# Kernel tuning notes

Measured on AMD Instinct MI355X. Metric: run time of the kernel, lower is better.

Reference implementation:

```python
import jax, jax.numpy as jnp
import numpy as np
import math

B, N, DIM = 4, 4096, 1024
HEADS, DHEAD, NRF = 16, 64, 64
STAB = 1e-6  # numerical_stabilizer


def setup_inputs() -> dict:
    key = jax.random.key(0)
    k1, k2, k3, k4 = jax.random.split(key, 4)
    x = jax.random.normal(k1, (B, N, DIM), dtype=jnp.float32)
    W_qkv = jax.random.normal(k2, (DIM, 3 * HEADS * DHEAD), dtype=jnp.float32) * (1.0 / math.sqrt(DIM))
    RF = jax.random.normal(k3, (HEADS, DHEAD, NRF), dtype=jnp.float32) / math.sqrt(NRF)
    W_out = jax.random.normal(k4, (HEADS * DHEAD, DIM), dtype=jnp.float32) * (1.0 / math.sqrt(HEADS * DHEAD))
    b_out = jnp.zeros((DIM,), dtype=jnp.float32)
    return {"x": x, "W_qkv": W_qkv, "RF": RF, "W_out": W_out, "b_out": b_out}


def _phi(t, RF):
    # kernel transformation: project onto random features, then ReLU (default kernel)
    return jax.nn.relu(jnp.einsum('bhnd,hdr->bhnr', t, RF))


def reference(x, W_qkv, RF, W_out, b_out):
    b, n, _ = x.shape
    qkv = x @ W_qkv                                  # [b, n, 3*h*d]
    q, k, v = jnp.split(qkv, 3, axis=-1)
    def to_heads(t):
        return t.reshape(b, n, HEADS, DHEAD).transpose(0, 2, 1, 3)  # [b,h,n,d]
    q, k, v = to_heads(q), to_heads(k), to_heads(v)

    phi_q = _phi(q, RF)                              # [b,h,n,r]
    phi_k = _phi(k, RF)                              # [b,h,n,r]

    # linear-complexity FAVOR+ attention
    kv = jnp.einsum('bhnr,bhnd->bhrd', phi_k, v)     # [b,h,r,d]
    out = jnp.einsum('bhnr,bhrd->bhnd', phi_q, kv)   # [b,h,n,d]
    # normalizer: einsum('bhnr,bhmr->bhn') == phi_q @ sum_m(phi_k)
    k_sum = phi_k.sum(axis=2)                        # [b,h,r]
    normalizer = jnp.einsum('bhnr,bhr->bhn', phi_q, k_sum)[..., None] + STAB
    out = out / normalizer

    out = out.transpose(0, 2, 1, 3).reshape(b, n, HEADS * DHEAD)
    out = out @ W_out + b_out
    return out
```

## Files before the change

### kernel.cpp

```cpp
#include <hip/hip_runtime.h>


typedef __attribute__((ext_vector_type(8))) short s8v;
typedef __attribute__((ext_vector_type(4))) short s4v;
typedef __attribute__((ext_vector_type(4))) float f4v;
typedef __attribute__((ext_vector_type(4))) int   i4v;

#define MFMA16(a, b, c) __builtin_amdgcn_mfma_f32_16x16x32_bf16((a), (b), (c), 0, 0, 0)

__device__ __forceinline__ unsigned short f2bf(float f) {
  unsigned int u = __builtin_bit_cast(unsigned int, f);
  unsigned int r = (u + 0x7FFFu + ((u >> 16) & 1u)) >> 16;
  return (unsigned short)r;
}

__device__ __forceinline__ int swz(int p) {
  return p ^ (((p >> 7) & 7) << 4);
}
__device__ __forceinline__ int swz8(int p) {
  return p ^ (((p >> 8) & 7) << 4);
}

__device__ __forceinline__ void gl_lds16(const void* g, void* l) {
  __builtin_amdgcn_global_load_lds(
      (const __attribute__((address_space(1))) void*)g,
      (__attribute__((address_space(3))) void*)l, 16, 0, 0);
}

__global__ __launch_bounds__(256) void cvt_bf16(const float* __restrict__ in,
                                                unsigned short* __restrict__ out,
                                                int n4) {
  int i = blockIdx.x * 256 + threadIdx.x;
  if (i >= n4) return;
  f4v v = ((const f4v*)in)[i];
  s4v o;
#pragma unroll
  for (int j = 0; j < 4; ++j) o[j] = (short)f2bf(v[j]);
  ((s4v*)out)[i] = o;
}

__global__ __launch_bounds__(256) void transpose_cvt(const float* __restrict__ in,
                                                     unsigned short* __restrict__ out,
                                                     int R, int C) {
  __shared__ float tile[32][33];
  const int tx = threadIdx.x, ty = threadIdx.y;
  const int c0 = blockIdx.x * 32, r0 = blockIdx.y * 32;
#pragma unroll
  for (int j = 0; j < 4; ++j)
    tile[ty + j * 8][tx] = in[(size_t)(r0 + ty + j * 8) * C + c0 + tx];
  __syncthreads();
#pragma unroll
  for (int j = 0; j < 4; ++j)
    out[(size_t)(c0 + ty + j * 8) * R + r0 + tx] = f2bf(tile[tx][ty + j * 8]);
}

__global__ __launch_bounds__(256) void fold_w(const float* __restrict__ W_qkv,
                                              const float* __restrict__ RF,
                                              unsigned short* __restrict__ wqkvt) {
  __shared__ float RFl[64 * 64];
  __shared__ float Wl[128 * 65];
  const int t = threadIdx.x;
  const int k0 = blockIdx.x * 128, h = blockIdx.y, part = blockIdx.z;
#pragma unroll
  for (int i = 0; i < 16; ++i) RFl[i * 256 + t] = RF[h * 4096 + i * 256 + t];
#pragma unroll
  for (int i = 0; i < 32; ++i) {
    int idx = i * 256 + t, kk = idx >> 6, d = idx & 63;
    Wl[kk * 65 + d] = W_qkv[(size_t)(k0 + kk) * 3072 + part * 1024 + h * 64 + d];
  }
  __syncthreads();
  const int w = t >> 6, lane = t & 63;
  const int rg = w >> 1;
  const int kk = (w & 1) * 64 + lane;
#pragma unroll
  for (int j = 0; j < 32; ++j) {
    const int r = rg * 32 + j;
    float s = 0.f;
#pragma unroll
    for (int d = 0; d < 64; ++d) s += Wl[kk * 65 + d] * RFl[d * 64 + r];
    wqkvt[(size_t)(part * 1024 + h * 64 + r) * 1024 + k0 + kk] = f2bf(s);
  }
}

template <int MODE>
__global__ __launch_bounds__(512, 2) void gemm256(const unsigned short* __restrict__ A,
                                                  const unsigned short* __restrict__ Bt,
                                                  void* __restrict__ Cout,
                                                  unsigned short* __restrict__ kT,
                                                  unsigned short* __restrict__ vT,
                                                  const float* __restrict__ bias,
                                                  int Nn, int K, int NTN, int CPX) {
  __shared__ __align__(128) unsigned short smem[65536];
  const int t = threadIdx.x, w = t >> 6, lane = t & 63;
  const int wm = w >> 2, wn = w & 3;
  const int fr = lane & 15, c16 = (lane >> 4) * 16;
  const int nkt = K >> 6;

  const int bid = blockIdx.x;
  const int wg = (bid & 7) * CPX + (bid >> 3);
  const int tm = wg / NTN, tn = wg % NTN;

  const unsigned short* gA = A + (size_t)tm * 256 * K;
  const unsigned short* gB = Bt + (size_t)tn * 256 * K;

  const int s0 = swz(t * 16);
  const int s1 = swz(8192 + t * 16);
  const int goff0 = (s0 >> 7) * K + ((s0 & 127) >> 1);
  const int goff1 = ((s1 - 8192) >> 7) * K + ((s1 & 127) >> 1) + 64 * K;
  const int woff = w * 1024;

  auto stage = [&](int T2, int part) {
    if (T2 >= nkt) return;
    char* reg = (char*)smem + (((T2 & 1) * 4 + part) << 14);
    const unsigned short* gp =
        (part < 2 ? gA : gB) + (size_t)((part & 1) * 128) * K + T2 * 64;
    gl_lds16(gp + goff0, reg + woff);
    gl_lds16(gp + goff1, reg + 8192 + woff);
  };

  f4v acc[8][4] = {};
  stage(0, 0); stage(0, 1); stage(0, 2); stage(0, 3);

  auto rdA = [&](int mh, s8v (&a)[4][2], const char* Ar) {
#pragma unroll
    for (int i = 0; i < 4; ++i)
#pragma unroll
      for (int ks = 0; ks < 2; ++ks) {
        int p = swz((mh * 64 + i * 16 + fr) * 128 + ks * 64 + c16);
        a[i][ks] = *(const s8v*)(Ar + p);
      }
  };
  auto rdB = [&](int nh, s8v (&b)[2][2], const char* Br, int brow) {
#pragma unroll
    for (int j = 0; j < 2; ++j)
#pragma unroll
      for (int ks = 0; ks < 2; ++ks) {
        int p = swz((brow + nh * 32 + j * 16 + fr) * 128 + ks * 64 + c16);
        b[j][ks] = *(const s8v*)(Br + p);
      }
  };
  auto mmac = [&](int mh, int nh, const s8v (&a)[4][2], const s8v (&b)[2][2]) {
    __builtin_amdgcn_s_setprio(1);
#pragma unroll
    for (int i = 0; i < 4; ++i)
#pragma unroll
      for (int j = 0; j < 2; ++j) {
        acc[mh * 4 + i][nh * 2 + j] = MFMA16(a[i][0], b[j][0], acc[mh * 4 + i][nh * 2 + j]);
        acc[mh * 4 + i][nh * 2 + j] = MFMA16(a[i][1], b[j][1], acc[mh * 4 + i][nh * 2 + j]);
      }
    __builtin_amdgcn_s_setprio(0);
  };

  const int brow = (wn & 1) * 64;
  for (int T = 0; T < nkt; ++T) {
    const int d = T & 1;
    const char* Ar = (const char*)smem + ((d * 4 + wm) << 14);
    const char* Br = (const char*)smem + ((d * 4 + 2 + (wn >> 1)) << 14);
    asm volatile("s_waitcnt vmcnt(0)" ::: "memory");
    __builtin_amdgcn_s_barrier();
    __builtin_amdgcn_sched_barrier(0);
    stage(T + 1, 0); stage(T + 1, 1); stage(T + 1, 2); stage(T + 1, 3);
    s8v a[4][2], b0[2][2], b1[2][2];
    rdA(0, a, Ar); rdB(0, b0, Br, brow); rdB(1, b1, Br, brow);
    mmac(0, 0, a, b0);
    mmac(0, 1, a, b1);
    rdA(1, a, Ar);
    mmac(1, 1, a, b1);
    mmac(1, 0, a, b0);
  }

  const int sec = tn >> 2;
#pragma unroll
  for (int m = 0; m < 8; ++m)
#pragma unroll
    for (int n = 0; n < 4; ++n) {
      const int row = tm * 256 + wm * 128 + m * 16 + (lane >> 4) * 4;
      const int col = tn * 256 + wn * 64 + n * 16 + fr;
      if (MODE == 0) {
        if (sec == 0) {
          unsigned short* C = (unsigned short*)Cout;
#pragma unroll
          for (int r = 0; r < 4; ++r)
            C[(size_t)(row + r) * 1024 + col] = f2bf(fmaxf(acc[m][n][r], 0.0f));
        } else {
          const int cl = col & 1023;
          const int bh = (row >> 12) * 16 + (cl >> 6);
          unsigned short* T = (sec == 1) ? kT : vT;
          s4v o;
#pragma unroll
          for (int g = 0; g < 4; ++g)
            o[g] = (short)f2bf(sec == 1 ? fmaxf(acc[m][n][g], 0.0f) : acc[m][n][g]);
          *(s4v*)&T[((size_t)bh * 64 + (cl & 63)) * 4096 + (row & 4095)] = o;
        }
      } else {
        float* C = (float*)Cout;
        const float bv = bias[col];
#pragma unroll
        for (int r = 0; r < 4; ++r)
          C[(size_t)(row + r) * Nn + col] = acc[m][n][r] + bv;
      }
    }
}

__global__ __launch_bounds__(256) void kv_gemm(const unsigned short* __restrict__ kT,
                                               const unsigned short* __restrict__ vT,
                                               float* __restrict__ kvpart) {
  __shared__ __align__(128) char lds[2 * 36864];
  const int t = threadIdx.x, w = t >> 6, lane = t & 63;
  const int och = blockIdx.x, bh = blockIdx.y;
  const int fr = lane & 15, c16 = (lane >> 4) * 16;
  const char* kTb = (const char*)kT + (size_t)bh * 64 * 8192 + och * 1024;
  const char* vTb = (const char*)vT + (size_t)bh * 64 * 8192 + och * 1024;

  for (int i = t; i < 2 * 2048; i += 256) {
    int buf = i >> 11, e = i & 2047;
    int row = 64 + (e >> 7), c = e & 127;
    int p = swz8(row * 256 + c * 2);
    *(unsigned short*)&lds[buf * 36864 + 16384 + p] = (row == 64) ? 0x3F80 : 0;
  }

  int srcoff[4];
#pragma unroll
  for (int i = 0; i < 4; ++i) {
    int p = swz8((i * 256 + t) * 16);
    srcoff[i] = (p >> 8) * 8192 + (p & 255);
  }
  auto stage = [&](int s) {
    if (s >= 4) return;
    char* base = lds + (s & 1) * 36864;
#pragma unroll
    for (int i = 0; i < 4; ++i) {
      gl_lds16(kTb + s * 256 + srcoff[i], base + (i * 256 + w * 64) * 16);
      gl_lds16(vTb + s * 256 + srcoff[i], base + 16384 + (i * 256 + w * 64) * 16);
    }
  };

  f4v kvacc[5] = {};
  stage(0);
  for (int s = 0; s < 4; ++s) {
    asm volatile("s_waitcnt vmcnt(0)" ::: "memory");
    __builtin_amdgcn_s_barrier();
    __builtin_amdgcn_sched_barrier(0);
    stage(s + 1);
    const char* kB = lds + (s & 1) * 36864;
    const char* vB = kB + 16384;
    s8v a[4];
#pragma unroll
    for (int ks = 0; ks < 4; ++ks)
      a[ks] = *(const s8v*)(kB + swz8((w * 16 + fr) * 256 + ks * 64 + c16));
    __builtin_amdgcn_s_setprio(1);
#pragma unroll
    for (int f = 0; f < 5; ++f) {
#pragma unroll
      for (int ks = 0; ks < 4; ++ks) {
        s8v b = *(const s8v*)(vB + swz8((f * 16 + fr) * 256 + ks * 64 + c16));
        kvacc[f] = MFMA16(a[ks], b, kvacc[f]);
      }
    }
    __builtin_amdgcn_s_setprio(0);
  }
  float* outp = kvpart + ((size_t)bh * 8 + och) * (80 * 64);
#pragma unroll
  for (int f = 0; f < 5; ++f)
    *(f4v*)&outp[(f * 16 + fr) * 64 + w * 16 + (lane >> 4) * 4] = kvacc[f];
}

__global__ __launch_bounds__(256) void kv_reduce(const float* __restrict__ kvpart,
                                                 unsigned short* __restrict__ kvt) {
  const int bh = blockIdx.x, t = threadIdx.x;
  for (int i = t; i < 80 * 64; i += 256) {
    float s = 0.f;
#pragma unroll
    for (int c = 0; c < 8; ++c) s += kvpart[((size_t)bh * 8 + c) * 5120 + i];
    kvt[(size_t)bh * 5120 + i] = f2bf(s);
  }
}

__global__ __launch_bounds__(256) void phiq_out(const unsigned short* __restrict__ phiq,
                                                const unsigned short* __restrict__ kvt,
                                                unsigned short* __restrict__ attno) {
  __shared__ __align__(128) unsigned short phl[128 * 64];
  __shared__ unsigned short kvl[80 * 72];
  const int t = threadIdx.x, w = t >> 6, lane = t & 63;
  const int ch = blockIdx.x, h = blockIdx.y, b = blockIdx.z;
  const int fr = lane & 15, kg = (lane >> 4) * 8, c16 = (lane >> 4) * 16;
  const int bh = b * 16 + h;
  const size_t rowbase = (size_t)(b * 4096 + ch * 128);
  const char* src = (const char*)phiq + rowbase * 2048 + h * 128;

#pragma unroll
  for (int i = 0; i < 4; ++i) {
    int p = swz((i * 256 + t) * 16);
    gl_lds16(src + (p >> 7) * 2048 + (p & 127),
             (char*)phl + (i * 256 + w * 64) * 16);
  }
  for (int i = t; i < 640; i += 256) {
    int row = i >> 3, cg = (i & 7) * 8;
    *(i4v*)&kvl[row * 72 + cg] = *(const i4v*)&kvt[(size_t)bh * 5120 + row * 64 + cg];
  }
  __syncthreads();

  f4v acc[2][5] = {};
#pragma unroll
  for (int ks = 0; ks < 2; ++ks) {
    s8v pa[2], kb[5];
#pragma unroll
    for (int m = 0; m < 2; ++m)
      pa[m] = *(const s8v*)((const char*)phl +
                            swz((w * 32 + m * 16 + fr) * 128 + ks * 64 + c16));
#pragma unroll
    for (int f = 0; f < 5; ++f)
      kb[f] = *(const s8v*)&kvl[(f * 16 + fr) * 72 + ks * 32 + kg];
#pragma unroll
    for (int m = 0; m < 2; ++m)
#pragma unroll
      for (int f = 0; f < 5; ++f) acc[m][f] = MFMA16(pa[m], kb[f], acc[m][f]);
  }
#pragma unroll
  for (int m = 0; m < 2; ++m)
#pragma unroll
    for (int g = 0; g < 4; ++g) {
      float nrm = __shfl(acc[m][4][g], lane & 48) + 1e-6f;
      int n = w * 32 + m * 16 + (lane >> 4) * 4 + g;
      size_t orow = rowbase + n;
#pragma unroll
      for (int f = 0; f < 4; ++f)
        attno[orow * 1024 + h * 64 + f * 16 + fr] = f2bf(acc[m][f][g] / nrm);
    }
}

extern "C" void kernel_launch(void* const* d_in, const int* in_sizes, int n_in,
                              void* d_out, int out_size, void* d_ws, size_t ws_size,
                              hipStream_t stream) {
  const float* x = (const float*)d_in[0];
  const float* W_qkv = (const float*)d_in[1];
  const float* RF = (const float*)d_in[2];
  const float* W_out = (const float*)d_in[3];
  const float* b_out = (const float*)d_in[4];
  float* out = (float*)d_out;

  char* ws = (char*)d_ws;
  size_t off = 0;
  auto alloc = [&](size_t bytes) -> void* {
    void* p = ws + off;
    off += (bytes + 255) & ~(size_t)255;
    return p;
  };
  unsigned short* xb = (unsigned short*)alloc(16384ull * 1024 * 2);
  unsigned short* wqkvt = (unsigned short*)alloc(3072ull * 1024 * 2);
  unsigned short* woutt = (unsigned short*)alloc(1024ull * 1024 * 2);
  unsigned short* phiq = (unsigned short*)alloc(16384ull * 1024 * 2);
  unsigned short* kT = (unsigned short*)alloc(64ull * 64 * 4096 * 2);
  unsigned short* vT = (unsigned short*)alloc(64ull * 64 * 4096 * 2);
  float* kvpart = (float*)alloc(64ull * 8 * 80 * 64 * 4);
  unsigned short* kvt = (unsigned short*)alloc(64ull * 80 * 64 * 2);
  unsigned short* attno = (unsigned short*)alloc(16384ull * 1024 * 2);

  cvt_bf16<<<16384, 256, 0, stream>>>(x, xb, 4194304);
  transpose_cvt<<<dim3(96, 32), dim3(32, 8), 0, stream>>>(W_qkv, wqkvt, 1024, 3072);
  transpose_cvt<<<dim3(32, 32), dim3(32, 8), 0, stream>>>(W_out, woutt, 1024, 1024);
  fold_w<<<dim3(8, 16, 2), 256, 0, stream>>>(W_qkv, RF, wqkvt);

  gemm256<0><<<768, 512, 0, stream>>>(xb, wqkvt, phiq, kT, vT, nullptr,
                                      3072, 1024, 12, 96);
  kv_gemm<<<dim3(8, 64), 256, 0, stream>>>(kT, vT, kvpart);
  kv_reduce<<<64, 256, 0, stream>>>(kvpart, kvt);
  phiq_out<<<dim3(32, 16, 4), 256, 0, stream>>>(phiq, kvt, attno);
  gemm256<1><<<256, 512, 0, stream>>>(attno, woutt, out, nullptr, nullptr, b_out,
                                      1024, 1024, 4, 32);
}
```

Before: 260.4 us.

## Store QKV GEMM output row-major and transpose phi_k/v in kv kernel via LDS

The QKV GEMM epilogue no longer scatters phi_k and v into transposed per-head buffers. It now writes all three sections row-major into one combined buffer, with ReLU applied to the first two sections. The kv kernel now loads phi_k and v rows from that buffer into registers and transposes them through padded LDS before the MFMA. This replaces the async global-to-LDS double-buffered pipeline with synchronous loads and scalar LDS transposes. The transpose_cvt launch for W_qkv is also narrowed to the v columns, since fold_w overwrites the q/k parts.

After: 256.9 us. Within noise of the previous version (-1.4%).

```diff
diff --git a/kernel.cpp b/kernel.cpp
--- a/kernel.cpp
+++ b/kernel.cpp
@@ -16,9 +16,6 @@
 
 __device__ __forceinline__ int swz(int p) {
   return p ^ (((p >> 7) & 7) << 4);
-}
-__device__ __forceinline__ int swz8(int p) {
-  return p ^ (((p >> 8) & 7) << 4);
 }
 
 __device__ __forceinline__ void gl_lds16(const void* g, void* l) {
@@ -86,8 +83,6 @@
 __global__ __launch_bounds__(512, 2) void gemm256(const unsigned short* __restrict__ A,
                                                   const unsigned short* __restrict__ Bt,
                                                   void* __restrict__ Cout,
-                                                  unsigned short* __restrict__ kT,
-                                                  unsigned short* __restrict__ vT,
                                                   const float* __restrict__ bias,
                                                   int Nn, int K, int NTN, int CPX) {
   __shared__ __align__(128) unsigned short smem[65536];
@@ -169,7 +164,7 @@
     mmac(1, 0, a, b0);
   }
 
-  const int sec = tn >> 2;
+  const bool rel = (MODE == 0) && (tn < 8);
 #pragma unroll
   for (int m = 0; m < 8; ++m)
 #pragma unroll
@@ -177,20 +172,11 @@
       const int row = tm * 256 + wm * 128 + m * 16 + (lane >> 4) * 4;
       const int col = tn * 256 + wn * 64 + n * 16 + fr;
       if (MODE == 0) {
-        if (sec == 0) {
-          unsigned short* C = (unsigned short*)Cout;
-#pragma unroll
-          for (int r = 0; r < 4; ++r)
-            C[(size_t)(row + r) * 1024 + col] = f2bf(fmaxf(acc[m][n][r], 0.0f));
-        } else {
-          const int cl = col & 1023;
-          const int bh = (row >> 12) * 16 + (cl >> 6);
-          unsigned short* T = (sec == 1) ? kT : vT;
-          s4v o;
-#pragma unroll
-          for (int g = 0; g < 4; ++g)
-            o[g] = (short)f2bf(sec == 1 ? fmaxf(acc[m][n][g], 0.0f) : acc[m][n][g]);
-          *(s4v*)&T[((size_t)bh * 64 + (cl & 63)) * 4096 + (row & 4095)] = o;
+        unsigned short* C = (unsigned short*)Cout;
+#pragma unroll
+        for (int r = 0; r < 4; ++r) {
+          float v = acc[m][n][r];
+          C[(size_t)(row + r) * Nn + col] = f2bf(rel ? fmaxf(v, 0.0f) : v);
         }
       } else {
         float* C = (float*)Cout;
@@ -202,67 +188,62 @@
     }
 }
 
-__global__ __launch_bounds__(256) void kv_gemm(const unsigned short* __restrict__ kT,
-                                               const unsigned short* __restrict__ vT,
+__global__ __launch_bounds__(256) void phik_kv(const unsigned short* __restrict__ phib,
                                                float* __restrict__ kvpart) {
-  __shared__ __align__(128) char lds[2 * 36864];
+  __shared__ unsigned short pkt[64 * 136];
+  __shared__ unsigned short vt[80 * 136];
   const int t = threadIdx.x, w = t >> 6, lane = t & 63;
-  const int och = blockIdx.x, bh = blockIdx.y;
-  const int fr = lane & 15, c16 = (lane >> 4) * 16;
-  const char* kTb = (const char*)kT + (size_t)bh * 64 * 8192 + och * 1024;
-  const char* vTb = (const char*)vT + (size_t)bh * 64 * 8192 + och * 1024;
-
-  for (int i = t; i < 2 * 2048; i += 256) {
-    int buf = i >> 11, e = i & 2047;
-    int row = 64 + (e >> 7), c = e & 127;
-    int p = swz8(row * 256 + c * 2);
-    *(unsigned short*)&lds[buf * 36864 + 16384 + p] = (row == 64) ? 0x3F80 : 0;
-  }
-
-  int srcoff[4];
-#pragma unroll
-  for (int i = 0; i < 4; ++i) {
-    int p = swz8((i * 256 + t) * 16);
-    srcoff[i] = (p >> 8) * 8192 + (p & 255);
-  }
-  auto stage = [&](int s) {
-    if (s >= 4) return;
-    char* base = lds + (s & 1) * 36864;
-#pragma unroll
-    for (int i = 0; i < 4; ++i) {
-      gl_lds16(kTb + s * 256 + srcoff[i], base + (i * 256 + w * 64) * 16);
-      gl_lds16(vTb + s * 256 + srcoff[i], base + 16384 + (i * 256 + w * 64) * 16);
-    }
-  };
+  const int och = blockIdx.x, h = blockIdx.y, b = blockIdx.z;
+  const int fr = lane & 15, kg = (lane >> 4) * 8;
+
+  for (int i = t; i < 136; i += 256) vt[64 * 136 + i] = 0x3F80;
+  for (int i = t; i < 15 * 136; i += 256) vt[65 * 136 + i] = 0;
 
   f4v kvacc[5] = {};
-  stage(0);
-  for (int s = 0; s < 4; ++s) {
-    asm volatile("s_waitcnt vmcnt(0)" ::: "memory");
-    __builtin_amdgcn_s_barrier();
-    __builtin_amdgcn_sched_barrier(0);
-    stage(s + 1);
-    const char* kB = lds + (s & 1) * 36864;
-    const char* vB = kB + 16384;
-    s8v a[4];
-#pragma unroll
-    for (int ks = 0; ks < 4; ++ks)
-      a[ks] = *(const s8v*)(kB + swz8((w * 16 + fr) * 256 + ks * 64 + c16));
-    __builtin_amdgcn_s_setprio(1);
-#pragma unroll
-    for (int f = 0; f < 5; ++f) {
-#pragma unroll
-      for (int ks = 0; ks < 4; ++ks) {
-        s8v b = *(const s8v*)(vB + swz8((f * 16 + fr) * 256 + ks * 64 + c16));
-        kvacc[f] = MFMA16(a[ks], b, kvacc[f]);
-      }
-    }
-    __builtin_amdgcn_s_setprio(0);
-  }
+  for (int c = 0; c < 4; ++c) {
+    const size_t rowbase = (size_t)(b * 4096 + och * 512 + c * 128);
+    i4v kreg[4], vreg[4];
+#pragma unroll
+    for (int it = 0; it < 4; ++it) {
+      int slot = it * 256 + t;
+      const unsigned short* rp =
+          &phib[(rowbase + (slot >> 3)) * 3072 + h * 64 + (slot & 7) * 8];
+      kreg[it] = *(const i4v*)(rp + 1024);
+      vreg[it] = *(const i4v*)(rp + 2048);
+    }
+    __syncthreads();
+#pragma unroll
+    for (int it = 0; it < 4; ++it) {
+      int slot = it * 256 + t;
+      int vn = slot >> 3, c8 = (slot & 7) * 8;
+      const unsigned short* kr = (const unsigned short*)&kreg[it];
+      const unsigned short* vr = (const unsigned short*)&vreg[it];
+#pragma unroll
+      for (int j = 0; j < 8; ++j) {
+        pkt[(c8 + j) * 136 + vn] = kr[j];
+        vt[(c8 + j) * 136 + vn] = vr[j];
+      }
+    }
+    __syncthreads();
+#pragma unroll
+    for (int kst = 0; kst < 4; ++kst) {
+      s8v pb = *(const s8v*)&pkt[(w * 16 + fr) * 136 + kst * 32 + kg];
+#pragma unroll
+      for (int f = 0; f < 5; ++f) {
+        s8v va = *(const s8v*)&vt[(f * 16 + fr) * 136 + kst * 32 + kg];
+        kvacc[f] = MFMA16(va, pb, kvacc[f]);
+      }
+    }
+  }
+  const int bh = b * 16 + h;
   float* outp = kvpart + ((size_t)bh * 8 + och) * (80 * 64);
 #pragma unroll
-  for (int f = 0; f < 5; ++f)
-    *(f4v*)&outp[(f * 16 + fr) * 64 + w * 16 + (lane >> 4) * 4] = kvacc[f];
+  for (int f = 0; f < 5; ++f) {
+    int row = f * 16 + (lane >> 4) * 4;
+    int col = w * 16 + fr;
+#pragma unroll
+    for (int g = 0; g < 4; ++g) outp[(row + g) * 64 + col] = kvacc[f][g];
+  }
 }
 
 __global__ __launch_bounds__(256) void kv_reduce(const float* __restrict__ kvpart,
@@ -276,7 +257,7 @@
   }
 }
 
-__global__ __launch_bounds__(256) void phiq_out(const unsigned short* __restrict__ phiq,
+__global__ __launch_bounds__(256) void phiq_out(const unsigned short* __restrict__ phib,
                                                 const unsigned short* __restrict__ kvt,
                                                 unsigned short* __restrict__ attno) {
   __shared__ __align__(128) unsigned short phl[128 * 64];
@@ -286,12 +267,12 @@
   const int fr = lane & 15, kg = (lane >> 4) * 8, c16 = (lane >> 4) * 16;
   const int bh = b * 16 + h;
   const size_t rowbase = (size_t)(b * 4096 + ch * 128);
-  const char* src = (const char*)phiq + rowbase * 2048 + h * 128;
+  const char* src = (const char*)phib + rowbase * 6144 + h * 128;
 
 #pragma unroll
   for (int i = 0; i < 4; ++i) {
     int p = swz((i * 256 + t) * 16);
-    gl_lds16(src + (p >> 7) * 2048 + (p & 127),
+    gl_lds16(src + (p >> 7) * 6144 + (p & 127),
              (char*)phl + (i * 256 + w * 64) * 16);
   }
   for (int i = t; i < 640; i += 256) {
@@ -349,23 +330,20 @@
   unsigned short* xb = (unsigned short*)alloc(16384ull * 1024 * 2);
   unsigned short* wqkvt = (unsigned short*)alloc(3072ull * 1024 * 2);
   unsigned short* woutt = (unsigned short*)alloc(1024ull * 1024 * 2);
-  unsigned short* phiq = (unsigned short*)alloc(16384ull * 1024 * 2);
-  unsigned short* kT = (unsigned short*)alloc(64ull * 64 * 4096 * 2);
-  unsigned short* vT = (unsigned short*)alloc(64ull * 64 * 4096 * 2);
+  unsigned short* phib = (unsigned short*)alloc(16384ull * 3072 * 2);
   float* kvpart = (float*)alloc(64ull * 8 * 80 * 64 * 4);
   unsigned short* kvt = (unsigned short*)alloc(64ull * 80 * 64 * 2);
   unsigned short* attno = (unsigned short*)alloc(16384ull * 1024 * 2);
 
   cvt_bf16<<<16384, 256, 0, stream>>>(x, xb, 4194304);
-  transpose_cvt<<<dim3(96, 32), dim3(32, 8), 0, stream>>>(W_qkv, wqkvt, 1024, 3072);
+  transpose_cvt<<<dim3(32, 32), dim3(32, 8), 0, stream>>>(
+      W_qkv + 2048, wqkvt + 2048ull * 1024, 1024, 3072);
   transpose_cvt<<<dim3(32, 32), dim3(32, 8), 0, stream>>>(W_out, woutt, 1024, 1024);
   fold_w<<<dim3(8, 16, 2), 256, 0, stream>>>(W_qkv, RF, wqkvt);
 
-  gemm256<0><<<768, 512, 0, stream>>>(xb, wqkvt, phiq, kT, vT, nullptr,
-                                      3072, 1024, 12, 96);
-  kv_gemm<<<dim3(8, 64), 256, 0, stream>>>(kT, vT, kvpart);
+  gemm256<0><<<768, 512, 0, stream>>>(xb, wqkvt, phib, nullptr, 3072, 1024, 12, 96);
+  phik_kv<<<dim3(8, 16, 4), 256, 0, stream>>>(phib, kvpart);
   kv_reduce<<<64, 256, 0, stream>>>(kvpart, kvt);
-  phiq_out<<<dim3(32, 16, 4), 256, 0, stream>>>(phiq, kvt, attno);
-  gemm256<1><<<256, 512, 0, stream>>>(attno, woutt, out, nullptr, nullptr, b_out,
-                                      1024, 1024, 4, 32);
-}
+  phiq_out<<<dim3(32, 16, 4), 256, 0, stream>>>(phib, kvt, attno);
+  gemm256<1><<<256, 512, 0, stream>>>(attno, woutt, out, b_out, 1024, 1024, 4, 32);
+}
```
